# Kernel optimization log

Measured on AMD Instinct MI355X. Metric: run time of the kernel, lower is better.

The kernel has to match this reference:

```python
import jax, jax.numpy as jnp
import numpy as np

EMB = 768          # MineModel.emb_size
HEADS = 4          # Mi hard-codes n_heads=4 for QTLayer
DK = EMB // HEADS  # 192
H_NEED = 3         # MineModel need_num_heads
QLEN = 10000
TLEN = 3000
EG = 100000        # give edges (before head replication)
EI = 100000        # inter_1 / inter_2 edges
NLAYERS = 2


def setup_inputs() -> dict:
    key = jax.random.key(0)
    ks = jax.random.split(key, 20)
    f = lambda k, s: jax.random.normal(k, s, dtype=jnp.float32) * 0.02
    return {
        'q_emb': jax.random.normal(ks[0], (QLEN, EMB), jnp.float32),
        't_emb': jax.random.normal(ks[1], (TLEN, EMB), jnp.float32),
        'give_src': jax.random.randint(ks[2], (EG,), 0, TLEN),
        'give_dst': jax.random.randint(ks[3], (EG,), 0, QLEN),
        'i1_src': jax.random.randint(ks[4], (EI,), 0, TLEN),
        'i1_dst': jax.random.randint(ks[5], (EI,), 0, TLEN),
        'i2_src': jax.random.randint(ks[6], (EI,), 0, TLEN),
        'i2_dst': jax.random.randint(ks[7], (EI,), 0, TLEN),
        'Wq_enc': f(ks[8], (EMB, EMB * H_NEED)),
        'bq_enc': jnp.zeros((EMB * H_NEED,), jnp.float32),
        'Wc': f(ks[9], (EMB, 10)),
        'bc': jnp.zeros((10,), jnp.float32),
        'centers': f(ks[10], (10, EMB)),
        'kW': f(ks[11], (NLAYERS, 2, EMB, EMB)),
        'kb': jnp.zeros((NLAYERS, 2, EMB), jnp.float32),
        'qW': f(ks[12], (NLAYERS, 2, EMB, EMB)),
        'qb': jnp.zeros((NLAYERS, 2, EMB), jnp.float32),
        'vW': f(ks[13], (NLAYERS, 2, EMB, EMB)),
        'vb': jnp.zeros((NLAYERS, 2, EMB), jnp.float32),
        'rel_att': f(ks[14], (NLAYERS, 3, HEADS, DK, DK)),
        'rel_msg': f(ks[15], (NLAYERS, 3, HEADS, DK, DK)),
        'rel_pri': jnp.ones((NLAYERS, 3, HEADS), jnp.float32),
        'Wout': f(ks[16], (EMB, EMB)),
        'bout': jnp.zeros((EMB,), jnp.float32),
    }


def _edge_softmax(score, dst, n_dst):
    # softmax over incoming edges of each destination node, per head
    m = jax.ops.segment_max(score, dst, num_segments=n_dst)      # [N, H]
    e = jnp.exp(score - m[dst])
    s = jax.ops.segment_sum(e, dst, num_segments=n_dst)
    return e / s[dst]


def _rel(k_src, v_src, q_dst, src, dst, n_dst, ratt, rmsg, rpri):
    # HGT relation: relation-specific K/V transform, edge dot-attention, scatter-sum
    k = jnp.einsum('nhd,hde->nhe', k_src, ratt)                  # [Nsrc, H, DK]
    v = jnp.einsum('nhd,hde->nhe', v_src, rmsg)
    score = jnp.einsum('ehd,ehd->eh', q_dst[dst], k[src]) * rpri / jnp.sqrt(jnp.float32(DK))
    a = _edge_softmax(score, dst, n_dst)                         # [E, H]
    return jax.ops.segment_sum(v[src] * a[:, :, None], dst, num_segments=n_dst)


def reference(q_emb, t_emb, give_src, give_dst, i1_src, i1_dst, i2_src, i2_dst,
              Wq_enc, bq_enc, Wc, bc, centers, kW, kb, qW, qb, vW, vb,
              rel_att, rel_msg, rel_pri, Wout, bout):
    n_q = QLEN * H_NEED
    # replicate 'give' edges per model-level head (cached graph construction)
    g_src = jnp.tile(give_src, H_NEED)
    g_dst = jnp.concatenate([give_dst + QLEN * i for i in range(H_NEED)])

    # question encoder -> split heads along feature dim, concat along rows
    q_hs = q_emb @ Wq_enc + bq_enc                               # [Q, EMB*H]
    q_h = q_hs.reshape(QLEN, H_NEED, EMB).transpose(1, 0, 2).reshape(n_q, EMB)
    q_h = q_h + jnp.tile(q_emb, (H_NEED, 1))
    assign = jax.nn.softmax(q_h @ Wc + bc, axis=-1)              # [n_q, 10]
    q_h = q_h + assign @ centers

    h_tag, h_q = t_emb, q_h
    for l in range(NLAYERS):
        k_tag = (h_tag @ kW[l, 0] + kb[l, 0]).reshape(-1, HEADS, DK)
        v_tag = (h_tag @ vW[l, 0] + vb[l, 0]).reshape(-1, HEADS, DK)
        q_tag = (h_tag @ qW[l, 0] + qb[l, 0]).reshape(-1, HEADS, DK)
        q_que = (h_q @ qW[l, 1] + qb[l, 1]).reshape(-1, HEADS, DK)
        t_q = _rel(k_tag, v_tag, q_que, g_src, g_dst, n_q,
                   rel_att[l, 0], rel_msg[l, 0], rel_pri[l, 0])
        t1 = _rel(k_tag, v_tag, q_tag, i1_src, i1_dst, TLEN,
                  rel_att[l, 1], rel_msg[l, 1], rel_pri[l, 1])
        t2 = _rel(k_tag, v_tag, q_tag, i2_src, i2_dst, TLEN,
                  rel_att[l, 2], rel_msg[l, 2], rel_pri[l, 2])
        # cross_reducer='mean' over the two tag->tag relations; residual add
        h_tag = (0.5 * (t1 + t2)).reshape(-1, EMB) + h_tag
        h_q = t_q.reshape(-1, EMB) + h_q

    ques_heads = h_q @ Wout + bout                               # [H*Q, EMB]
    tags = h_tag @ Wout + bout                                   # [T, EMB]
    # torch.split(.., q_len, dim=0) + stack(dim=1) -> [Q, H, EMB]
    ques = ques_heads.reshape(H_NEED, QLEN, EMB).transpose(1, 0, 2)
    return ques, tags
```

## Files before the change

kernel.cpp:

```cpp
#include <hip/hip_runtime.h>

#define QLEN 10000
#define TLEN 3000
#define EMB 768
#define HNEED 3
#define NQ (QLEN * HNEED)
#define EG 100000
#define EI 100000
#define DKH 192
#define NHEADS 4

namespace {

typedef unsigned short u16;
typedef unsigned char u8;
typedef unsigned int u32;
typedef __attribute__((ext_vector_type(8))) short bf16x8;
typedef __attribute__((ext_vector_type(4))) float f32x4;
typedef __attribute__((ext_vector_type(2))) float f32x2;

constexpr float SCALE = 0.07216878364870322f;

__device__ inline u16 f2bf(float f) {
  unsigned u = __float_as_uint(f);
  unsigned r = (u + 0x7FFFu + ((u >> 16) & 1u)) >> 16;
  return (u16)r;
}
__device__ inline float bf2f(u16 h) {
  return __uint_as_float((unsigned)h << 16);
}
__device__ inline u8 f2fp8(float f) {
  u32 pk = __builtin_amdgcn_cvt_pk_fp8_f32(f, f, 0, false);
  return (u8)(pk & 0xFF);
}
__device__ inline void decode12(const u32* p, float* o) {
#pragma unroll
  for (int t = 0; t < 3; ++t) {
    u32 w = p[t];
    f32x2 lo = __builtin_amdgcn_cvt_pk_f32_fp8(w, false);
    f32x2 hi = __builtin_amdgcn_cvt_pk_f32_fp8(w, true);
    o[t * 4 + 0] = lo[0]; o[t * 4 + 1] = lo[1];
    o[t * 4 + 2] = hi[0]; o[t * 4 + 3] = hi[1];
  }
}
__device__ inline f32x2 bfx2(u32 w) {
  f32x2 r;
  r[0] = __uint_as_float(w << 16);
  r[1] = __uint_as_float(w & 0xFFFF0000u);
  return r;
}

__device__ inline void gload_lds16(const u16* g, u16* s) {
  __builtin_amdgcn_global_load_lds(
      (const __attribute__((address_space(1))) unsigned*)g,
      (__attribute__((address_space(3))) unsigned*)s, 16, 0, 0);
}

template <int EPI, int OUT>
__global__ __launch_bounds__(256) void gemm_bf16(
    const u16* __restrict__ A, int lda, long long sAz,
    const u16* __restrict__ Bt, int ldb, long long sBz,
    void* __restrict__ Cv, int ldc, long long sCz, long long sCz2, int relpack,
    const float* __restrict__ bias, const float* __restrict__ extra,
    int M, int N, int K)
{
  __shared__ __align__(16) u16 As[2][4096];
  __shared__ __align__(16) u16 Bs[2][4096];
  const int z = blockIdx.z;
  float* Cf = (float*)Cv;
  u16* Ch = (u16*)Cv;
  u8* C8 = (u8*)Cv;
  if (relpack) {
    const int zr = z >> 3, zh = z & 7;
    A += (long long)zh * sAz;
    Bt += (long long)z * sBz;
    const long long co = (long long)zr * sCz2 + (long long)zh * sCz;
    Cf += co; Ch += co; C8 += co;
  } else {
    A += (long long)z * sAz;
    Bt += (long long)z * sBz;
    Cf += (long long)z * sCz;
    Ch += (long long)z * sCz;
    C8 += (long long)z * sCz;
  }
  const int gx = gridDim.x;
  const int nwg = gx * gridDim.y;
  const int orig = blockIdx.y * gx + blockIdx.x;
  const int qq = nwg >> 3, rr = nwg & 7;
  const int xc = orig & 7, ix = orig >> 3;
  const int swz = (xc < rr ? xc * (qq + 1) : rr * (qq + 1) + (xc - rr) * qq) + ix;
  const int by = swz / gx, bx = swz - by * gx;
  const int bm = by * 128, bn = bx * 128;

  const int tid = threadIdx.x;
  const int w = tid >> 6, l = tid & 63;
  const int wr = w >> 1, wc = w & 1;
  const int l16 = l & 15, lk = l >> 4;
  const int srow = tid >> 2;
  const int scol = (((tid & 3) ^ ((srow >> 1) & 3))) * 8;
  const int rchunk = (lk ^ ((l16 >> 1) & 3));

  int r0 = bm + srow;      if (r0 > M - 1) r0 = M - 1;
  int r1 = bm + srow + 64; if (r1 > M - 1) r1 = M - 1;
  int c0 = bn + srow;      if (c0 > N - 1) c0 = N - 1;
  int c1 = bn + srow + 64; if (c1 > N - 1) c1 = N - 1;
  const u16* pa0 = A + (long long)r0 * lda + scol;
  const u16* pa1 = A + (long long)r1 * lda + scol;
  const u16* pb0 = Bt + (long long)c0 * ldb + scol;
  const u16* pb1 = Bt + (long long)c1 * ldb + scol;

  f32x4 acc[4][4] = {};
  const int nt = K / 32;

  auto stage = [&](int buf, int k0) {
    gload_lds16(pa0 + k0, &As[buf][w * 512]);
    gload_lds16(pa1 + k0, &As[buf][w * 512 + 2048]);
    gload_lds16(pb0 + k0, &Bs[buf][w * 512]);
    gload_lds16(pb1 + k0, &Bs[buf][w * 512 + 2048]);
  };

  stage(0, 0);
  __syncthreads();
  int cur = 0;
  for (int t = 0; t < nt; ++t) {
    if (t + 1 < nt) stage(cur ^ 1, (t + 1) * 32);
    bf16x8 af[4], bf[4];
#pragma unroll
    for (int m = 0; m < 4; ++m)
      af[m] = *(const bf16x8*)&As[cur][(wr * 64 + m * 16 + l16) * 32 + rchunk * 8];
#pragma unroll
    for (int n = 0; n < 4; ++n)
      bf[n] = *(const bf16x8*)&Bs[cur][(wc * 64 + n * 16 + l16) * 32 + rchunk * 8];
#pragma unroll
    for (int m = 0; m < 4; ++m)
#pragma unroll
      for (int n = 0; n < 4; ++n)
        acc[m][n] = __builtin_amdgcn_mfma_f32_16x16x32_bf16(af[m], bf[n], acc[m][n], 0, 0, 0);
    __syncthreads();
    cur ^= 1;
  }

#pragma unroll
  for (int m = 0; m < 4; ++m) {
#pragma unroll
    for (int j = 0; j < 4; ++j) {
      int grow = bm + wr * 64 + m * 16 + lk * 4 + j;
      if (grow >= M) continue;
#pragma unroll
      for (int n = 0; n < 4; ++n) {
        int gcol = bn + wc * 64 + n * 16 + l16;
        if (gcol >= N) continue;
        float val = acc[m][n][j] + (bias ? bias[gcol] : 0.f);
        if (EPI == 0) {
          if (OUT == 0)
            Cf[(long long)grow * ldc + gcol] = val;
          else if (OUT == 1)
            Ch[(long long)grow * ldc + gcol] = f2bf(val);
          else
            C8[(long long)grow * ldc + gcol] = f2fp8(val);
        } else if (EPI == 1) {
          int h = gcol / EMB, c = gcol - h * EMB;
          Ch[((long long)h * QLEN + grow) * EMB + c] =
              f2bf(val + extra[(long long)grow * EMB + c]);
        } else {
          int i2 = grow % QLEN, h = grow / QLEN;
          Cf[((long long)i2 * HNEED + h) * EMB + gcol] = val;
        }
      }
    }
  }
}

__global__ void f2bf_kernel(const float* __restrict__ in, u16* __restrict__ out, long long n)
{
  long long i = ((long long)blockIdx.x * 256 + threadIdx.x) * 4;
  if (i >= n) return;
  float4 v = *(const float4*)(in + i);
  ushort4 o;
  o.x = f2bf(v.x); o.y = f2bf(v.y); o.z = f2bf(v.z); o.w = f2bf(v.w);
  *(ushort4*)(out + i) = o;
}

__global__ __launch_bounds__(256) void transpose_bf(
    const float* __restrict__ in, u16* __restrict__ out, int R, int C, int G, int OG)
{
  __shared__ float t[32][33];
  const int z = blockIdx.z;
  in += (long long)z * R * C;
  out += (long long)((z / G) * OG + (z % G)) * R * C;
  const int c0 = blockIdx.x * 32, r0 = blockIdx.y * 32;
  const int tx = threadIdx.x & 31, ty = threadIdx.x >> 5;
  for (int i = 0; i < 32; i += 8) {
    int r = r0 + ty + i, c = c0 + tx;
    t[ty + i][tx] = (r < R && c < C) ? in[(long long)r * C + c] : 0.f;
  }
  __syncthreads();
  for (int i = 0; i < 32; i += 8) {
    int c = c0 + ty + i, r = r0 + tx;
    if (c < C && r < R) out[(long long)c * R + r] = f2bf(t[tx][ty + i]);
  }
}

__global__ void pack_wct_kernel(const float* __restrict__ Wc, float* __restrict__ WcT)
{
  int idx = blockIdx.x * 256 + threadIdx.x;
  if (idx >= 7680) return;
  int j = idx / EMB, d = idx - j * EMB;
  WcT[idx] = Wc[d * 10 + j];
}

__global__ void pack_bias_kernel(const float* __restrict__ kb, const float* __restrict__ vb,
                                 const float* __restrict__ qb, float* __restrict__ o)
{
  int idx = blockIdx.x * 256 + threadIdx.x;
  if (idx >= 2 * 2304) return;
  int l = idx / 2304, c = idx - l * 2304;
  float v;
  if (c < 768) v = kb[(l * 2) * EMB + c];
  else if (c < 1536) v = vb[(l * 2) * EMB + c - 768];
  else v = qb[(l * 2) * EMB + c - 1536];
  o[idx] = v;
}

__global__ __launch_bounds__(512) void assign_center512(
    u16* __restrict__ qh_bf,
    const float* __restrict__ WcT, const float* __restrict__ bc,
    const float* __restrict__ centers)
{
  __shared__ float wc_s[7680];
  __shared__ float cen_s[7680];
  const int tid = threadIdx.x;
  for (int i = tid; i < 7680; i += 512) {
    wc_s[i] = WcT[i];
    cen_s[i] = centers[i];
  }
  __syncthreads();
  const int wave = tid >> 6, lane = tid & 63;
  const int row = blockIdx.x * 8 + wave;
  const long long base = (long long)row * EMB;
  float x[12];
#pragma unroll
  for (int i = 0; i < 12; ++i) x[i] = bf2f(qh_bf[base + lane + 64 * i]);
  float part[10] = {};
#pragma unroll
  for (int i = 0; i < 12; ++i) {
    const float v = x[i];
    const int d = lane + 64 * i;
#pragma unroll
    for (int j = 0; j < 10; ++j) part[j] = fmaf(v, wc_s[j * EMB + d], part[j]);
  }
#pragma unroll
  for (int j = 0; j < 10; ++j)
#pragma unroll
    for (int off = 32; off; off >>= 1) part[j] += __shfl_xor(part[j], off);
  float mx = -1e30f;
#pragma unroll
  for (int j = 0; j < 10; ++j) { part[j] += bc[j]; mx = fmaxf(mx, part[j]); }
  float s = 0.f;
#pragma unroll
  for (int j = 0; j < 10; ++j) { part[j] = __expf(part[j] - mx); s += part[j]; }
  const float inv = 1.f / s;
#pragma unroll
  for (int i = 0; i < 12; ++i) {
    const int d = lane + 64 * i;
    float acc = 0.f;
#pragma unroll
    for (int j = 0; j < 10; ++j) acc = fmaf(part[j], cen_s[j * EMB + d], acc);
    qh_bf[base + d] = f2bf(x[i] + acc * inv);
  }
}

__global__ void hist_kernel(const int* __restrict__ dst, int* __restrict__ cnt, int E)
{
  int e = blockIdx.x * 256 + threadIdx.x;
  if (e < E) atomicAdd(&cnt[dst[e]], 1);
}

__global__ __launch_bounds__(1024) void scan_fill_kernel(
    const int* __restrict__ cnt, int* __restrict__ rowptr, int* __restrict__ cur, int n)
{
  __shared__ int buf[1024];
  const int tid = threadIdx.x;
  const int chunk = (n + 1023) >> 10;
  const int base = tid * chunk;
  int s = 0;
  for (int i = 0; i < chunk; ++i) {
    int idx = base + i;
    if (idx < n) s += cnt[idx];
  }
  buf[tid] = s;
  __syncthreads();
  for (int off = 1; off < 1024; off <<= 1) {
    int v = (tid >= off) ? buf[tid - off] : 0;
    __syncthreads();
    buf[tid] += v;
    __syncthreads();
  }
  int run = (tid == 0) ? 0 : buf[tid - 1];
  for (int i = 0; i < chunk; ++i) {
    int idx = base + i;
    if (idx < n) {
      rowptr[idx] = run;
      cur[idx] = run;
      run += cnt[idx];
    }
  }
  if (tid == 1023) rowptr[n] = buf[1023];
}

__global__ void fill_kernel(const int* __restrict__ src, const int* __restrict__ dst,
                            int* __restrict__ cur, int* __restrict__ adj, int E)
{
  int e = blockIdx.x * 256 + threadIdx.x;
  if (e < E) {
    int p = atomicAdd(&cur[dst[e]], 1);
    adj[p] = src[e];
  }
}

__global__ __launch_bounds__(256) void gather_give(
    const u8* __restrict__ q, const u8* __restrict__ kv,
    const int* __restrict__ rowptr, const int* __restrict__ adj,
    const float* __restrict__ rpri, u16* __restrict__ hq_bf)
{
  const int d = (blockIdx.x * 256 + threadIdx.x) >> 6;
  const int lane = threadIdx.x & 63;
  if (d >= QLEN) return;
  const int rs = rowptr[d], re = rowptr[d + 1];
  if (rs == re) return;
  const int h = lane >> 4, sub = lane & 15;
  const int off = h * DKH + sub * 12;
  const float pri = rpri[h] * SCALE;

  float qv[3][12];
#pragma unroll
  for (int c = 0; c < 3; ++c)
    decode12((const u32*)(q + (size_t)(c * QLEN + d) * EMB + off), qv[c]);

  float S[3] = {0.f, 0.f, 0.f};
  float A[3][12] = {};

  auto edge = [&](int sn) {
    float kf[12], vf[12];
    decode12((const u32*)(kv + (size_t)sn * 1536 + off), kf);
    decode12((const u32*)(kv + (size_t)sn * 1536 + 768 + off), vf);
    float dt[3] = {0.f, 0.f, 0.f};
#pragma unroll
    for (int t = 0; t < 12; ++t) {
#pragma unroll
      for (int c = 0; c < 3; ++c) dt[c] = fmaf(qv[c][t], kf[t], dt[c]);
    }
#pragma unroll
    for (int c = 0; c < 3; ++c) {
#pragma unroll
      for (int o2 = 8; o2; o2 >>= 1) dt[c] += __shfl_xor(dt[c], o2);
      const float e = __expf(dt[c] * pri);
      S[c] += e;
#pragma unroll
      for (int t = 0; t < 12; ++t) A[c][t] = fmaf(e, vf[t], A[c][t]);
    }
  };
  int i = rs;
  for (; i + 1 < re; i += 2) { edge(adj[i]); edge(adj[i + 1]); }
  if (i < re) edge(adj[i]);

#pragma unroll
  for (int c = 0; c < 3; ++c) {
    const float inv = 1.f / S[c];
    u32* o = (u32*)(hq_bf + (size_t)(c * QLEN + d) * EMB + off);
#pragma unroll
    for (int t = 0; t < 6; ++t) {
      f32x2 r = bfx2(o[t]);
      r[0] += A[c][2 * t] * inv;
      r[1] += A[c][2 * t + 1] * inv;
      o[t] = (u32)f2bf(r[0]) | ((u32)f2bf(r[1]) << 16);
    }
  }
}

__global__ __launch_bounds__(256) void gather_inter(
    const u16* __restrict__ tag_kvq,
    const u8* __restrict__ kv1, const u8* __restrict__ kv2,
    const int* __restrict__ rp1, const int* __restrict__ adj1,
    const int* __restrict__ rp2, const int* __restrict__ adj2,
    const float* __restrict__ pri1, const float* __restrict__ pri2,
    u16* __restrict__ htag_bf)
{
  const int d = (blockIdx.x * 256 + threadIdx.x) >> 6;
  const int lane = threadIdx.x & 63;
  if (d >= TLEN) return;
  const int rs1 = rp1[d], re1 = rp1[d + 1];
  const int rs2 = rp2[d], re2 = rp2[d + 1];
  if (rs1 == re1 && rs2 == re2) return;
  const int h = lane >> 4, sub = lane & 15;
  const int off = h * DKH + sub * 12;
  float qv[12];
  {
    const u32* qp = (const u32*)(tag_kvq + (size_t)d * 2304 + 1536 + off);
#pragma unroll
    for (int t = 0; t < 6; ++t) {
      f32x2 r = bfx2(qp[t]);
      qv[2 * t] = r[0]; qv[2 * t + 1] = r[1];
    }
  }
  float R[12] = {};
#pragma unroll
  for (int rel = 0; rel < 2; ++rel) {
    const u8* kv = rel ? kv2 : kv1;
    const int rs = rel ? rs2 : rs1, re = rel ? re2 : re1;
    const int* adj = rel ? adj2 : adj1;
    if (rs == re) continue;
    const float pri = (rel ? pri2[h] : pri1[h]) * SCALE;
    float S = 0.f, A[12] = {};
    auto edge = [&](int sn) {
      float kf[12], vf[12];
      decode12((const u32*)(kv + (size_t)sn * 1536 + off), kf);
      decode12((const u32*)(kv + (size_t)sn * 1536 + 768 + off), vf);
      float dt = 0.f;
#pragma unroll
      for (int t = 0; t < 12; ++t) dt = fmaf(qv[t], kf[t], dt);
#pragma unroll
      for (int o2 = 8; o2; o2 >>= 1) dt += __shfl_xor(dt, o2);
      const float e = __expf(dt * pri);
      S += e;
#pragma unroll
      for (int t = 0; t < 12; ++t) A[t] = fmaf(e, vf[t], A[t]);
    };
    int i = rs;
    for (; i + 1 < re; i += 2) { edge(adj[i]); edge(adj[i + 1]); }
    if (i < re) edge(adj[i]);
    const float inv = 0.5f / S;
#pragma unroll
    for (int t = 0; t < 12; ++t) R[t] = fmaf(A[t], inv, R[t]);
  }
  u32* o = (u32*)(htag_bf + (size_t)d * EMB + off);
#pragma unroll
  for (int t = 0; t < 6; ++t) {
    f32x2 r = bfx2(o[t]);
    r[0] += R[2 * t];
    r[1] += R[2 * t + 1];
    o[t] = (u32)f2bf(r[0]) | ((u32)f2bf(r[1]) << 16);
  }
}

}

extern "C" void kernel_launch(void* const* d_in, const int* in_sizes, int n_in,
                              void* d_out, int out_size, void* d_ws, size_t ws_size,
                              hipStream_t stream)
{
  const float* q_emb   = (const float*)d_in[0];
  const float* t_emb   = (const float*)d_in[1];
  const int*   give_src = (const int*)d_in[2];
  const int*   give_dst = (const int*)d_in[3];
  const int*   i1_src  = (const int*)d_in[4];
  const int*   i1_dst  = (const int*)d_in[5];
  const int*   i2_src  = (const int*)d_in[6];
  const int*   i2_dst  = (const int*)d_in[7];
  const float* Wq_enc  = (const float*)d_in[8];
  const float* bq_enc  = (const float*)d_in[9];
  const float* Wc      = (const float*)d_in[10];
  const float* bc      = (const float*)d_in[11];
  const float* centers = (const float*)d_in[12];
  const float* kW      = (const float*)d_in[13];
  const float* kb      = (const float*)d_in[14];
  const float* qW      = (const float*)d_in[15];
  const float* qb      = (const float*)d_in[16];
  const float* vW      = (const float*)d_in[17];
  const float* vb      = (const float*)d_in[18];
  const float* rel_att = (const float*)d_in[19];
  const float* rel_msg = (const float*)d_in[20];
  const float* rel_pri = (const float*)d_in[21];
  const float* Wout    = (const float*)d_in[22];
  const float* bout    = (const float*)d_in[23];
  float* out = (float*)d_out;

  const long long WS = (long long)EMB * EMB;
  const long long RS = (long long)DKH * DKH;

  float* p = (float*)d_ws;
  auto take = [&](size_t n) { float* r = p; p += ((n + 3) & ~(size_t)3); return r; };
  u16* h_q_bf    = (u16*)take((size_t)NQ * EMB / 2);
  u16* h_tag_bf  = (u16*)take((size_t)TLEN * EMB / 2);
  u16* q_emb_bf  = (u16*)take((size_t)QLEN * EMB / 2);
  u16* tag_kvq   = (u16*)take((size_t)TLEN * 2304 / 2);
  u8* kv_all     = (u8*)take((size_t)3 * TLEN * 1536 / 4);
  u8* kv_g = kv_all;
  u8* kv_1 = kv_all + (size_t)TLEN * 1536;
  u8* kv_2 = kv_all + (size_t)2 * TLEN * 1536;
  u16* WqT   = (u16*)take((size_t)EMB * EMB * HNEED / 2);
  u16* qWT   = (u16*)take((size_t)4 * WS / 2);
  u16* Wtag  = (u16*)take((size_t)2 * 3 * WS / 2);
  u16* WoutT = (u16*)take((size_t)WS / 2);
  u16* relWT = (u16*)take((size_t)48 * RS / 2);
  float* WcT   = take(7680);
  float* b_kvq = take(2 * 2304);
  int* rp_g  = (int*)take(QLEN + 1);
  int* rp_1  = (int*)take(TLEN + 1);
  int* rp_2  = (int*)take(TLEN + 1);
  int* cur_g = (int*)take(QLEN);
  int* cur_1 = (int*)take(TLEN);
  int* cur_2 = (int*)take(TLEN);
  int* adj_g = (int*)take(EG);
  int* adj_1 = (int*)take(EI);
  int* adj_2 = (int*)take(EI);
  int* cnt   = (int*)take(QLEN);
  u8* q_que = (u8*)out;

  auto gemmb = [&](int EPI, int OUT, const u16* A, int lda, long long sAz,
                   const u16* Bt, int ldb, long long sBz,
                   void* C, int ldc, long long sCz, long long sCz2, int relpack,
                   const float* bias, const float* extra,
                   int M, int N, int K, int batch) {
    dim3 grid((N + 127) / 128, (M + 127) / 128, batch);
    if (EPI == 0 && OUT == 0)
      gemm_bf16<0, 0><<<grid, 256, 0, stream>>>(A, lda, sAz, Bt, ldb, sBz, C, ldc, sCz, sCz2, relpack, bias, extra, M, N, K);
    else if (EPI == 0 && OUT == 1)
      gemm_bf16<0, 1><<<grid, 256, 0, stream>>>(A, lda, sAz, Bt, ldb, sBz, C, ldc, sCz, sCz2, relpack, bias, extra, M, N, K);
    else if (EPI == 0 && OUT == 2)
      gemm_bf16<0, 2><<<grid, 256, 0, stream>>>(A, lda, sAz, Bt, ldb, sBz, C, ldc, sCz, sCz2, relpack, bias, extra, M, N, K);
    else if (EPI == 1)
      gemm_bf16<1, 1><<<grid, 256, 0, stream>>>(A, lda, sAz, Bt, ldb, sBz, C, ldc, sCz, sCz2, relpack, bias, extra, M, N, K);
    else
      gemm_bf16<2, 0><<<grid, 256, 0, stream>>>(A, lda, sAz, Bt, ldb, sBz, C, ldc, sCz, sCz2, relpack, bias, extra, M, N, K);
  };

  auto build_csr = [&](const int* src, const int* dst, int E, int n,
                       int* rp, int* cu, int* adj) {
    hipMemsetAsync(cnt, 0, (size_t)n * sizeof(int), stream);
    hist_kernel<<<(E + 255) / 256, 256, 0, stream>>>(dst, cnt, E);
    scan_fill_kernel<<<1, 1024, 0, stream>>>(cnt, rp, cu, n);
    fill_kernel<<<(E + 255) / 256, 256, 0, stream>>>(src, dst, cu, adj, E);
  };
  build_csr(give_src, give_dst, EG, QLEN, rp_g, cur_g, adj_g);
  build_csr(i1_src, i1_dst, EI, TLEN, rp_1, cur_1, adj_1);
  build_csr(i2_src, i2_dst, EI, TLEN, rp_2, cur_2, adj_2);

  pack_wct_kernel<<<30, 256, 0, stream>>>(Wc, WcT);
  pack_bias_kernel<<<18, 256, 0, stream>>>(kb, vb, qb, b_kvq);
  transpose_bf<<<dim3(EMB * HNEED / 32, EMB / 32, 1), 256, 0, stream>>>(Wq_enc, WqT, EMB, EMB * HNEED, 1, 1);
  transpose_bf<<<dim3(EMB / 32, EMB / 32, 4), 256, 0, stream>>>(qW, qWT, EMB, EMB, 1, 1);
  for (int l = 0; l < 2; ++l) {
    transpose_bf<<<dim3(EMB / 32, EMB / 32, 1), 256, 0, stream>>>(kW + (l * 2) * WS, Wtag + (l * 3 + 0) * WS, EMB, EMB, 1, 1);
    transpose_bf<<<dim3(EMB / 32, EMB / 32, 1), 256, 0, stream>>>(vW + (l * 2) * WS, Wtag + (l * 3 + 1) * WS, EMB, EMB, 1, 1);
    transpose_bf<<<dim3(EMB / 32, EMB / 32, 1), 256, 0, stream>>>(qW + (l * 2) * WS, Wtag + (l * 3 + 2) * WS, EMB, EMB, 1, 1);
  }
  transpose_bf<<<dim3(EMB / 32, EMB / 32, 1), 256, 0, stream>>>(Wout, WoutT, EMB, EMB, 1, 1);
  transpose_bf<<<dim3(DKH / 32, DKH / 32, 24), 256, 0, stream>>>(rel_att, relWT, DKH, DKH, 4, 8);
  transpose_bf<<<dim3(DKH / 32, DKH / 32, 24), 256, 0, stream>>>(rel_msg, relWT + 4 * RS, DKH, DKH, 4, 8);

  f2bf_kernel<<<(QLEN * EMB / 4 + 255) / 256, 256, 0, stream>>>(q_emb, q_emb_bf, (long long)QLEN * EMB);
  gemmb(1, 1, q_emb_bf, EMB, 0, WqT, EMB, 0, h_q_bf, EMB, 0, 0, 0, bq_enc, q_emb,
        QLEN, EMB * HNEED, EMB, 1);
  assign_center512<<<NQ / 8, 512, 0, stream>>>(h_q_bf, WcT, bc, centers);
  f2bf_kernel<<<(TLEN * EMB / 4 + 255) / 256, 256, 0, stream>>>(t_emb, h_tag_bf, (long long)TLEN * EMB);

  const long long KVZ = (long long)TLEN * 1536;
  for (int l = 0; l < 2; ++l) {
    gemmb(0, 1, h_tag_bf, EMB, 0, Wtag + (long long)l * 3 * WS, EMB, 0,
          tag_kvq, 2304, 0, 0, 0, b_kvq + l * 2304, nullptr, TLEN, 2304, EMB, 1);
    gemmb(0, 2, h_q_bf, EMB, 0, qWT + (l * 2 + 1) * WS, EMB, 0,
          q_que, EMB, 0, 0, 0, qb + (l * 2 + 1) * EMB, nullptr, NQ, EMB, EMB, 1);
    gemmb(0, 2, tag_kvq, 2304, 192, relWT + (long long)(l * 3) * 8 * RS, DKH, RS,
          kv_g, 1536, 192, KVZ, 1, nullptr, nullptr, TLEN, DKH, DKH, 24);
    gather_give<<<(QLEN * 64 + 255) / 256, 256, 0, stream>>>(
        q_que, kv_g, rp_g, adj_g, rel_pri + (l * 3 + 0) * NHEADS, h_q_bf);
    gather_inter<<<(TLEN * 64 + 255) / 256, 256, 0, stream>>>(
        tag_kvq, kv_1, kv_2, rp_1, adj_1, rp_2, adj_2,
        rel_pri + (l * 3 + 1) * NHEADS, rel_pri + (l * 3 + 2) * NHEADS,
        h_tag_bf);
  }

  gemmb(2, 0, h_q_bf, EMB, 0, WoutT, EMB, 0, out, EMB, 0, 0, 0, bout, nullptr,
        NQ, EMB, EMB, 1);
  gemmb(0, 0, h_tag_bf, EMB, 0, WoutT, EMB, 0, out + (size_t)NQ * EMB, EMB, 0, 0, 0,
        bout, nullptr, TLEN, EMB, EMB, 1);
}
```

Baseline: 882.0 us.

## Triple-buffer GEMM LDS staging with vmcnt waits and bf16 residual input

The bf16 GEMM moves from a double-buffered to a triple-buffered LDS pipeline that prefetches two K-tiles ahead. Explicit s_waitcnt vmcnt plus a single barrier per iteration replace the two __syncthreads. It also raises wave priority around the MFMA block and precomputes the LDS fragment offsets. The encoder residual now reads the bf16 copy of q_emb instead of fp32, halving that epilogue read at a small precision cost. LDS use grows to 48KB per block, which may reduce occupancy.

```diff
diff --git a/kernel.cpp b/kernel.cpp
--- a/kernel.cpp
+++ b/kernel.cpp
@@ -61,11 +61,11 @@
     const u16* __restrict__ A, int lda, long long sAz,
     const u16* __restrict__ Bt, int ldb, long long sBz,
     void* __restrict__ Cv, int ldc, long long sCz, long long sCz2, int relpack,
-    const float* __restrict__ bias, const float* __restrict__ extra,
+    const float* __restrict__ bias, const u16* __restrict__ extra,
     int M, int N, int K)
 {
-  __shared__ __align__(16) u16 As[2][4096];
-  __shared__ __align__(16) u16 Bs[2][4096];
+  __shared__ __align__(16) u16 As[3][4096];
+  __shared__ __align__(16) u16 Bs[3][4096];
   const int z = blockIdx.z;
   float* Cf = (float*)Cv;
   u16* Ch = (u16*)Cv;
@@ -109,6 +109,13 @@
   const u16* pb0 = Bt + (long long)c0 * ldb + scol;
   const u16* pb1 = Bt + (long long)c1 * ldb + scol;
 
+  int aoff[4], boff[4];
+#pragma unroll
+  for (int m = 0; m < 4; ++m) {
+    aoff[m] = (wr * 64 + m * 16 + l16) * 32 + rchunk * 8;
+    boff[m] = (wc * 64 + m * 16 + l16) * 32 + rchunk * 8;
+  }
+
   f32x4 acc[4][4] = {};
   const int nt = K / 32;
 
@@ -120,24 +127,34 @@
   };
 
   stage(0, 0);
-  __syncthreads();
-  int cur = 0;
+  stage(1, 32);
+  int cur = 0, sb = 2;
   for (int t = 0; t < nt; ++t) {
-    if (t + 1 < nt) stage(cur ^ 1, (t + 1) * 32);
+    if (t < nt - 1)
+      asm volatile("s_waitcnt vmcnt(4)" ::: "memory");
+    else
+      asm volatile("s_waitcnt vmcnt(0)" ::: "memory");
+    __builtin_amdgcn_s_barrier();
+    __builtin_amdgcn_sched_barrier(0);
+    if (t + 2 < nt) {
+      stage(sb, (t + 2) * 32);
+      if (++sb == 3) sb = 0;
+    }
     bf16x8 af[4], bf[4];
 #pragma unroll
     for (int m = 0; m < 4; ++m)
-      af[m] = *(const bf16x8*)&As[cur][(wr * 64 + m * 16 + l16) * 32 + rchunk * 8];
+      af[m] = *(const bf16x8*)&As[cur][aoff[m]];
 #pragma unroll
     for (int n = 0; n < 4; ++n)
-      bf[n] = *(const bf16x8*)&Bs[cur][(wc * 64 + n * 16 + l16) * 32 + rchunk * 8];
+      bf[n] = *(const bf16x8*)&Bs[cur][boff[n]];
+    __builtin_amdgcn_s_setprio(1);
 #pragma unroll
     for (int m = 0; m < 4; ++m)
 #pragma unroll
       for (int n = 0; n < 4; ++n)
         acc[m][n] = __builtin_amdgcn_mfma_f32_16x16x32_bf16(af[m], bf[n], acc[m][n], 0, 0, 0);
-    __syncthreads();
-    cur ^= 1;
+    __builtin_amdgcn_s_setprio(0);
+    if (++cur == 3) cur = 0;
   }
 
 #pragma unroll
@@ -161,7 +178,7 @@
         } else if (EPI == 1) {
           int h = gcol / EMB, c = gcol - h * EMB;
           Ch[((long long)h * QLEN + grow) * EMB + c] =
-              f2bf(val + extra[(long long)grow * EMB + c]);
+              f2bf(val + bf2f(extra[(long long)grow * EMB + c]));
         } else {
           int i2 = grow % QLEN, h = grow / QLEN;
           Cf[((long long)i2 * HNEED + h) * EMB + gcol] = val;
@@ -510,7 +527,7 @@
   auto gemmb = [&](int EPI, int OUT, const u16* A, int lda, long long sAz,
                    const u16* Bt, int ldb, long long sBz,
                    void* C, int ldc, long long sCz, long long sCz2, int relpack,
-                   const float* bias, const float* extra,
+                   const float* bias, const u16* extra,
                    int M, int N, int K, int batch) {
     dim3 grid((N + 127) / 128, (M + 127) / 128, batch);
     if (EPI == 0 && OUT == 0)
@@ -550,7 +567,7 @@
   transpose_bf<<<dim3(DKH / 32, DKH / 32, 24), 256, 0, stream>>>(rel_msg, relWT + 4 * RS, DKH, DKH, 4, 8);
 
   f2bf_kernel<<<(QLEN * EMB / 4 + 255) / 256, 256, 0, stream>>>(q_emb, q_emb_bf, (long long)QLEN * EMB);
-  gemmb(1, 1, q_emb_bf, EMB, 0, WqT, EMB, 0, h_q_bf, EMB, 0, 0, 0, bq_enc, q_emb,
+  gemmb(1, 1, q_emb_bf, EMB, 0, WqT, EMB, 0, h_q_bf, EMB, 0, 0, 0, bq_enc, q_emb_bf,
         QLEN, EMB * HNEED, EMB, 1);
   assign_center512<<<NQ / 8, 512, 0, stream>>>(h_q_bf, WcT, bc, centers);
   f2bf_kernel<<<(TLEN * EMB / 4 + 255) / 256, 256, 0, stream>>>(t_emb, h_tag_bf, (long long)TLEN * EMB);
```

Measured after the change: 877.9 us. No clear change (-0.5%).
